# Kernel optimization log

Hardware: AMD Instinct MI355X
Metric: run time of the kernel (lower is better)

The kernel has to match this reference:

```python
import jax, jax.numpy as jnp
import numpy as np

NUM_FEAS = 4096
HID = 128
BATCH = 128


def setup_inputs() -> dict:
    key = jax.random.key(0)
    k1, k2, k3, k4 = jax.random.split(key, 4)
    batch_x = jax.random.normal(k1, (BATCH, NUM_FEAS), dtype=jnp.float32)
    C = jax.random.normal(k2, (1, HID), dtype=jnp.float32)
    W = jax.random.normal(k3, (NUM_FEAS, HID), dtype=jnp.float32)
    B = jax.random.normal(k4, (NUM_FEAS,), dtype=jnp.float32)
    return {"batch_x": batch_x, "C": C, "W": W, "B": B}


def reference(batch_x, C, W, B):
    # binarize input (matches (x > 0).float())
    x = (batch_x > 0).astype(jnp.float32)  # [B, F]
    # prefix sums: S_excl[b, i] = sum_{j < i} x[b, j] * W[j]   -> [B, F, H]
    contrib = x[:, :, None] * W[None, :, :]
    S = jnp.cumsum(contrib, axis=1)
    S_excl = jnp.concatenate([jnp.zeros_like(S[:, :1]), S[:, :-1]], axis=1)
    # hidden state for i >= 1: h_i = sigmoid(S_excl_i + C)
    h = jax.nn.sigmoid(S_excl + C[None, :, :])  # [B, F, H]
    # faithful quirk: for i == 0 the original uses raw C (no sigmoid)
    h = h.at[:, 0, :].set(jnp.broadcast_to(C[0], (x.shape[0], HID)))
    # logits z_i = h_i . W_i + B_i ; p_i = sigmoid(z_i)
    z = jnp.einsum('bfh,fh->bf', h, W) + B[None, :]
    # BCE(sum over features), stable via log_sigmoid
    log_p = jax.nn.log_sigmoid(z)
    log_q = jax.nn.log_sigmoid(-z)
    loss_per_sample = -jnp.sum(x * log_p + (1.0 - x) * log_q, axis=1)
    return jnp.mean(loss_per_sample)
```

## Files before the change

kernel.cpp:

```cpp
#include <hip/hip_runtime.h>

#define NFEAS 4096
#define HID   128
#define BATCH 128
#define NSUB  64
#define NCH   16
#define KF    256
#define L2E   1.4426950408889634f
#define LN2   0.6931471805599453f

__device__ __forceinline__ float scan64(float v) {
  float r = v; int y;
  y = __builtin_amdgcn_update_dpp(0, __float_as_int(r), 0x111, 0xF, 0xF, true); r += __int_as_float(y);
  y = __builtin_amdgcn_update_dpp(0, __float_as_int(r), 0x112, 0xF, 0xF, true); r += __int_as_float(y);
  y = __builtin_amdgcn_update_dpp(0, __float_as_int(r), 0x114, 0xF, 0xF, true); r += __int_as_float(y);
  y = __builtin_amdgcn_update_dpp(0, __float_as_int(r), 0x118, 0xF, 0xF, true); r += __int_as_float(y);
  y = __builtin_amdgcn_update_dpp(0, __float_as_int(r), 0x142, 0xA, 0xF, true); r += __int_as_float(y);
  y = __builtin_amdgcn_update_dpp(0, __float_as_int(r), 0x143, 0xC, 0xF, true); r += __int_as_float(y);
  return r;
}

__device__ __forceinline__ void scan64_x4(float& a, float& b, float& c, float& d) {
  int t0, t1, t2, t3;
#define S4(ctrl, rm)                                                              \
  t0 = __builtin_amdgcn_update_dpp(0, __float_as_int(a), ctrl, rm, 0xF, true);    \
  t1 = __builtin_amdgcn_update_dpp(0, __float_as_int(b), ctrl, rm, 0xF, true);    \
  t2 = __builtin_amdgcn_update_dpp(0, __float_as_int(c), ctrl, rm, 0xF, true);    \
  t3 = __builtin_amdgcn_update_dpp(0, __float_as_int(d), ctrl, rm, 0xF, true);    \
  a += __int_as_float(t0); b += __int_as_float(t1);                               \
  c += __int_as_float(t2); d += __int_as_float(t3);
  S4(0x111, 0xF) S4(0x112, 0xF) S4(0x114, 0xF) S4(0x118, 0xF)
  S4(0x142, 0xA) S4(0x143, 0xC)
#undef S4
}

__global__ __launch_bounds__(128) void chunk_sums_kernel(
    const float* __restrict__ x, const float* __restrict__ W,
    float* __restrict__ T)
{
  __shared__ float xm[64][8];
  const int c = blockIdx.x, g = blockIdx.y, t = threadIdx.x;

  {
    const int s = t >> 4, fb = (t & 15) << 2;
    const float4 v = *reinterpret_cast<const float4*>(
        &x[(size_t)(g * 8 + s) * NFEAS + c * 64 + fb]);
    xm[fb + 0][s] = v.x > 0.f ? 1.f : 0.f;
    xm[fb + 1][s] = v.y > 0.f ? 1.f : 0.f;
    xm[fb + 2][s] = v.z > 0.f ? 1.f : 0.f;
    xm[fb + 3][s] = v.w > 0.f ? 1.f : 0.f;
  }
  __syncthreads();

  float acc[8];
  #pragma unroll
  for (int s = 0; s < 8; ++s) acc[s] = 0.f;

  #pragma unroll 4
  for (int f = 0; f < 64; ++f) {
    const float wv = W[(size_t)(c * 64 + f) * HID + t];
    const float4 ma = *reinterpret_cast<const float4*>(&xm[f][0]);
    const float4 mb = *reinterpret_cast<const float4*>(&xm[f][4]);
    acc[0] = __builtin_fmaf(ma.x, wv, acc[0]);
    acc[1] = __builtin_fmaf(ma.y, wv, acc[1]);
    acc[2] = __builtin_fmaf(ma.z, wv, acc[2]);
    acc[3] = __builtin_fmaf(ma.w, wv, acc[3]);
    acc[4] = __builtin_fmaf(mb.x, wv, acc[4]);
    acc[5] = __builtin_fmaf(mb.y, wv, acc[5]);
    acc[6] = __builtin_fmaf(mb.z, wv, acc[6]);
    acc[7] = __builtin_fmaf(mb.w, wv, acc[7]);
  }
  #pragma unroll
  for (int s = 0; s < 8; ++s)
    T[((size_t)(g * 8 + s) * HID + t) * NSUB + c] = acc[s];
}

__global__ __launch_bounds__(256) void prefix_s2m_kernel(
    const float* __restrict__ T, const float* __restrict__ Cv,
    float* __restrict__ s2m)
{
  const int gw = blockIdx.x * 4 + (threadIdx.x >> 6);
  const int lane = threadIdx.x & 63;
  const int h = gw & 127;
  const float v = T[(size_t)gw * NSUB + lane];
  const float r = scan64(v);
  if ((lane & 3) == 0) {
    const float excl = r - v;
    s2m[(size_t)(lane >> 2) * (BATCH * HID) + gw] = -L2E * (excl + Cv[h]);
  }
}

__global__ __launch_bounds__(512, 6) void zpart_kernel(
    const float* __restrict__ x,   const float* __restrict__ W,
    const float* __restrict__ Cv,  const float* __restrict__ s2m,
    float* __restrict__ zpart)
{
  __shared__ float wt[32 * 256];
  __shared__ float s2l[8 * 32];
  __shared__ float cvl[32];

  const int c  = blockIdx.x;
  const int hq = blockIdx.y;
  const int bg = blockIdx.z;
  const int tid = threadIdx.x, lane = tid & 63, w = tid >> 6;
  const int base = c * KF;

  {
    const int hb = tid & 7, f0 = tid >> 3;
    const float* wp = W + (size_t)(base + f0) * HID + (hq << 5) + (hb << 2);
    const int colw = f0 ^ ((hb & 3) << 3);
    #pragma unroll
    for (int k = 0; k < 4; ++k) {
      const float4 v = *reinterpret_cast<const float4*>(wp + (size_t)(k << 6) * HID);
      float* q = &wt[((hb << 2) << 8) + colw + (k << 6)];
      q[0] = v.x; q[256] = v.y; q[512] = v.z; q[768] = v.w;
    }
  }
  if (tid < 256) {
    s2l[tid] = s2m[(size_t)c * (BATCH * HID) +
                   (size_t)(bg * 8 + (tid >> 5)) * HID + (hq << 5) + (tid & 31)];
  }
  if (tid < 32) cvl[tid] = Cv[(hq << 5) + tid];
  __syncthreads();

  const int b = bg * 8 + w;
  const float4 xv = *reinterpret_cast<const float4*>(
      x + (size_t)b * NFEAS + base + (lane << 2));
  const float xm0 = xv.x > 0.f ? 1.f : 0.f;
  const float xm1 = xv.y > 0.f ? 1.f : 0.f;
  const float xm2 = xv.z > 0.f ? 1.f : 0.f;
  const float xm3 = xv.w > 0.f ? 1.f : 0.f;
  const bool qk = (c == 0) && (lane == 0);

  float z0 = 0.f, z1 = 0.f, z2 = 0.f, z3 = 0.f;

  #pragma unroll
  for (int cg = 0; cg < 8; ++cg) {
    const int colx = (lane << 2) ^ ((cg & 3) << 3);
    const int rb = (cg << 2) * 256 + colx;
    const float4 wv0 = *reinterpret_cast<const float4*>(&wt[rb]);
    const float4 wv1 = *reinterpret_cast<const float4*>(&wt[rb + 256]);
    const float4 wv2 = *reinterpret_cast<const float4*>(&wt[rb + 512]);
    const float4 wv3 = *reinterpret_cast<const float4*>(&wt[rb + 768]);

    const float m00 = wv0.x * xm0, m01 = wv0.y * xm1, m02 = wv0.z * xm2, m03 = wv0.w * xm3;
    const float m10 = wv1.x * xm0, m11 = wv1.y * xm1, m12 = wv1.z * xm2, m13 = wv1.w * xm3;
    const float m20 = wv2.x * xm0, m21 = wv2.y * xm1, m22 = wv2.z * xm2, m23 = wv2.w * xm3;
    const float m30 = wv3.x * xm0, m31 = wv3.y * xm1, m32 = wv3.z * xm2, m33 = wv3.w * xm3;

    const float ps0 = (m00 + m01) + (m02 + m03);
    const float ps1 = (m10 + m11) + (m12 + m13);
    const float ps2 = (m20 + m21) + (m22 + m23);
    const float ps3 = (m30 + m31) + (m32 + m33);

    float r0 = ps0, r1 = ps1, r2 = ps2, r3 = ps3;
    scan64_x4(r0, r1, r2, r3);

#define CHAIN(J, wvJ, rJ, psJ, mJ0, mJ1, mJ2)                                               \
    {                                                                                        \
      const int ch = (cg << 2) + J;                                                          \
      const float smJ = s2l[(w << 5) + ch];                                                  \
      const float e0 = rJ - psJ;                                                             \
      const float e1 = e0 + mJ0;                                                             \
      const float e2 = e1 + mJ1;                                                             \
      const float e3 = e2 + mJ2;                                                             \
      float g0 = __builtin_amdgcn_rcpf(1.f + __builtin_amdgcn_exp2f(__builtin_fmaf(e0, -L2E, smJ))); \
      const float g1 = __builtin_amdgcn_rcpf(1.f + __builtin_amdgcn_exp2f(__builtin_fmaf(e1, -L2E, smJ))); \
      const float g2 = __builtin_amdgcn_rcpf(1.f + __builtin_amdgcn_exp2f(__builtin_fmaf(e2, -L2E, smJ))); \
      const float g3 = __builtin_amdgcn_rcpf(1.f + __builtin_amdgcn_exp2f(__builtin_fmaf(e3, -L2E, smJ))); \
      if (qk) g0 = cvl[ch];                                   \
      z0 = __builtin_fmaf(g0, wvJ.x, z0);                                                    \
      z1 = __builtin_fmaf(g1, wvJ.y, z1);                                                    \
      z2 = __builtin_fmaf(g2, wvJ.z, z2);                                                    \
      z3 = __builtin_fmaf(g3, wvJ.w, z3);                                                    \
    }
    CHAIN(0, wv0, r0, ps0, m00, m01, m02)
    CHAIN(1, wv1, r1, ps1, m10, m11, m12)
    CHAIN(2, wv2, r2, ps2, m20, m21, m22)
    CHAIN(3, wv3, r3, ps3, m30, m31, m32)
#undef CHAIN
  }

  float4 zv; zv.x = z0; zv.y = z1; zv.z = z2; zv.w = z3;
  *reinterpret_cast<float4*>(
      &zpart[((size_t)hq * BATCH + b) * NFEAS + base + (lane << 2)]) = zv;
}

__global__ __launch_bounds__(256) void bce_kernel(
    const float* __restrict__ x, const float* __restrict__ Bv,
    const float* __restrict__ zpart, float* __restrict__ lossb)
{
  __shared__ float sm[256];
  const int b = blockIdx.x, t = threadIdx.x;
  const size_t Q = (size_t)BATCH * NFEAS;
  float acc = 0.f;
  #pragma unroll
  for (int i = 0; i < NFEAS / 256; ++i) {
    const int f = i * 256 + t;
    const size_t o = (size_t)b * NFEAS + f;
    const float zt = ((zpart[o] + zpart[Q + o]) +
                      (zpart[2 * Q + o] + zpart[3 * Q + o])) + Bv[f];
    const float xf = x[o] > 0.f ? 1.f : 0.f;
    const float az = __builtin_fabsf(zt);
    const float ee = __builtin_amdgcn_exp2f(-L2E * az);
    acc += fmaxf(zt, 0.f) - xf * zt + LN2 * __builtin_amdgcn_logf(1.f + ee);
  }
  sm[t] = acc;
  __syncthreads();
  for (int s = 128; s > 0; s >>= 1) {
    if (t < s) sm[t] += sm[t + s];
    __syncthreads();
  }
  if (t == 0) lossb[b] = sm[0];
}

__global__ __launch_bounds__(128) void finalize_kernel(
    const float* __restrict__ lossb, float* __restrict__ out)
{
  __shared__ float sm[128];
  const int t = threadIdx.x;
  sm[t] = lossb[t];
  __syncthreads();
  for (int s = 64; s > 0; s >>= 1) {
    if (t < s) sm[t] += sm[t + s];
    __syncthreads();
  }
  if (t == 0) out[0] = sm[0] * (1.f / BATCH);
}

extern "C" void kernel_launch(void* const* d_in, const int* in_sizes, int n_in,
                              void* d_out, int out_size, void* d_ws, size_t ws_size,
                              hipStream_t stream)
{
  const float* x  = (const float*)d_in[0];
  const float* Cv = (const float*)d_in[1];
  const float* W  = (const float*)d_in[2];
  const float* Bv = (const float*)d_in[3];
  float* out = (float*)d_out;

  float* T     = (float*)d_ws;
  float* s2m   = T     + (size_t)BATCH * HID * NSUB;
  float* zpart = s2m   + (size_t)NCH * BATCH * HID;
  float* lossb = zpart + (size_t)4 * BATCH * NFEAS;

  chunk_sums_kernel<<<dim3(NSUB, BATCH / 8), 128, 0, stream>>>(x, W, T);
  prefix_s2m_kernel<<<dim3(BATCH * HID / 4), 256, 0, stream>>>(T, Cv, s2m);
  zpart_kernel<<<dim3(NCH, 4, BATCH / 8), 512, 0, stream>>>(x, W, Cv, s2m, zpart);
  bce_kernel<<<dim3(BATCH), 256, 0, stream>>>(x, Bv, zpart, lossb);
  finalize_kernel<<<1, 128, 0, stream>>>(lossb, out);
}
```

Baseline: 57.68 us.

## Fuse hidden-quarter loop and BCE loss into z kernel with double-buffered W tiles

The z kernel now loops over all four hidden quarters inside one block, using double-buffered shared-memory W tiles with register prefetch, instead of launching one block per quarter. It then computes the BCE loss directly and reduces it per wave, which removes the zpart round trip through global memory and the separate bce kernel. The cost is a grid four times smaller (256 blocks of 512 threads) with more serial work per block, and lower occupancy from the larger shared footprint.

```diff
diff --git a/kernel.cpp b/kernel.cpp
--- a/kernel.cpp
+++ b/kernel.cpp
@@ -90,38 +90,46 @@
   }
 }
 
-__global__ __launch_bounds__(512, 6) void zpart_kernel(
+__global__ __launch_bounds__(512, 2) void zloss_kernel(
     const float* __restrict__ x,   const float* __restrict__ W,
     const float* __restrict__ Cv,  const float* __restrict__ s2m,
-    float* __restrict__ zpart)
-{
-  __shared__ float wt[32 * 256];
-  __shared__ float s2l[8 * 32];
-  __shared__ float cvl[32];
+    const float* __restrict__ Bv,  float* __restrict__ losses)
+{
+  __shared__ float wt[2][32 * 256];
+  __shared__ float s2l[8 * 128];
+  __shared__ float cvl[128];
 
   const int c  = blockIdx.x;
-  const int hq = blockIdx.y;
-  const int bg = blockIdx.z;
+  const int bg = blockIdx.y;
   const int tid = threadIdx.x, lane = tid & 63, w = tid >> 6;
   const int base = c * KF;
 
+  const int hb = tid & 7, f0s = tid >> 3;
+  const int colw = f0s ^ ((hb & 3) << 3);
+  const float* wp0 = W + (size_t)(base + f0s) * HID + (hb << 2);
+
+  float4 st0, st1, st2, st3;
+  st0 = *reinterpret_cast<const float4*>(wp0);
+  st1 = *reinterpret_cast<const float4*>(wp0 + (size_t)(1 << 6) * HID);
+  st2 = *reinterpret_cast<const float4*>(wp0 + (size_t)(2 << 6) * HID);
+  st3 = *reinterpret_cast<const float4*>(wp0 + (size_t)(3 << 6) * HID);
+
   {
-    const int hb = tid & 7, f0 = tid >> 3;
-    const float* wp = W + (size_t)(base + f0) * HID + (hq << 5) + (hb << 2);
-    const int colw = f0 ^ ((hb & 3) << 3);
-    #pragma unroll
-    for (int k = 0; k < 4; ++k) {
-      const float4 v = *reinterpret_cast<const float4*>(wp + (size_t)(k << 6) * HID);
-      float* q = &wt[((hb << 2) << 8) + colw + (k << 6)];
-      q[0] = v.x; q[256] = v.y; q[512] = v.z; q[768] = v.w;
-    }
-  }
-  if (tid < 256) {
-    s2l[tid] = s2m[(size_t)c * (BATCH * HID) +
-                   (size_t)(bg * 8 + (tid >> 5)) * HID + (hq << 5) + (tid & 31)];
-  }
-  if (tid < 32) cvl[tid] = Cv[(hq << 5) + tid];
-  __syncthreads();
+    const int s0i = tid, s1i = tid + 512;
+    s2l[s0i] = s2m[(size_t)c * (BATCH * HID) +
+                   (size_t)(bg * 8 + (s0i >> 7)) * HID + (s0i & 127)];
+    s2l[s1i] = s2m[(size_t)c * (BATCH * HID) +
+                   (size_t)(bg * 8 + (s1i >> 7)) * HID + (s1i & 127)];
+  }
+  if (tid < 128) cvl[tid] = Cv[tid];
+
+  {
+    float* q = &wt[0][((hb << 2) << 8) + colw];
+    q[0]       = st0.x; q[256]       = st0.y; q[512]       = st0.z; q[768]       = st0.w;
+    q[64]      = st1.x; q[64 + 256]  = st1.y; q[64 + 512]  = st1.z; q[64 + 768]  = st1.w;
+    q[128]     = st2.x; q[128 + 256] = st2.y; q[128 + 512] = st2.z; q[128 + 768] = st2.w;
+    q[192]     = st3.x; q[192 + 256] = st3.y; q[192 + 512] = st3.z; q[192 + 768] = st3.w;
+  }
 
   const int b = bg * 8 + w;
   const float4 xv = *reinterpret_cast<const float4*>(
@@ -134,95 +142,97 @@
 
   float z0 = 0.f, z1 = 0.f, z2 = 0.f, z3 = 0.f;
 
-  #pragma unroll
-  for (int cg = 0; cg < 8; ++cg) {
-    const int colx = (lane << 2) ^ ((cg & 3) << 3);
-    const int rb = (cg << 2) * 256 + colx;
-    const float4 wv0 = *reinterpret_cast<const float4*>(&wt[rb]);
-    const float4 wv1 = *reinterpret_cast<const float4*>(&wt[rb + 256]);
-    const float4 wv2 = *reinterpret_cast<const float4*>(&wt[rb + 512]);
-    const float4 wv3 = *reinterpret_cast<const float4*>(&wt[rb + 768]);
-
-    const float m00 = wv0.x * xm0, m01 = wv0.y * xm1, m02 = wv0.z * xm2, m03 = wv0.w * xm3;
-    const float m10 = wv1.x * xm0, m11 = wv1.y * xm1, m12 = wv1.z * xm2, m13 = wv1.w * xm3;
-    const float m20 = wv2.x * xm0, m21 = wv2.y * xm1, m22 = wv2.z * xm2, m23 = wv2.w * xm3;
-    const float m30 = wv3.x * xm0, m31 = wv3.y * xm1, m32 = wv3.z * xm2, m33 = wv3.w * xm3;
-
-    const float ps0 = (m00 + m01) + (m02 + m03);
-    const float ps1 = (m10 + m11) + (m12 + m13);
-    const float ps2 = (m20 + m21) + (m22 + m23);
-    const float ps3 = (m30 + m31) + (m32 + m33);
-
-    float r0 = ps0, r1 = ps1, r2 = ps2, r3 = ps3;
-    scan64_x4(r0, r1, r2, r3);
+  for (int hq = 0; hq < 4; ++hq) {
+    if (hq < 3) {
+      const float* wp = wp0 + ((hq + 1) << 5);
+      st0 = *reinterpret_cast<const float4*>(wp);
+      st1 = *reinterpret_cast<const float4*>(wp + (size_t)(1 << 6) * HID);
+      st2 = *reinterpret_cast<const float4*>(wp + (size_t)(2 << 6) * HID);
+      st3 = *reinterpret_cast<const float4*>(wp + (size_t)(3 << 6) * HID);
+    }
+    __syncthreads();
+    const float* wcur = wt[hq & 1];
+
+    #pragma unroll
+    for (int cg = 0; cg < 8; ++cg) {
+      const int colx = (lane << 2) ^ ((cg & 3) << 3);
+      const int rb = (cg << 2) * 256 + colx;
+      const float4 wv0 = *reinterpret_cast<const float4*>(&wcur[rb]);
+      const float4 wv1 = *reinterpret_cast<const float4*>(&wcur[rb + 256]);
+      const float4 wv2 = *reinterpret_cast<const float4*>(&wcur[rb + 512]);
+      const float4 wv3 = *reinterpret_cast<const float4*>(&wcur[rb + 768]);
+
+      const float m00 = wv0.x * xm0, m01 = wv0.y * xm1, m02 = wv0.z * xm2, m03 = wv0.w * xm3;
+      const float m10 = wv1.x * xm0, m11 = wv1.y * xm1, m12 = wv1.z * xm2, m13 = wv1.w * xm3;
+      const float m20 = wv2.x * xm0, m21 = wv2.y * xm1, m22 = wv2.z * xm2, m23 = wv2.w * xm3;
+      const float m30 = wv3.x * xm0, m31 = wv3.y * xm1, m32 = wv3.z * xm2, m33 = wv3.w * xm3;
+
+      const float ps0 = (m00 + m01) + (m02 + m03);
+      const float ps1 = (m10 + m11) + (m12 + m13);
+      const float ps2 = (m20 + m21) + (m22 + m23);
+      const float ps3 = (m30 + m31) + (m32 + m33);
+
+      float r0 = ps0, r1 = ps1, r2 = ps2, r3 = ps3;
+      scan64_x4(r0, r1, r2, r3);
 
 #define CHAIN(J, wvJ, rJ, psJ, mJ0, mJ1, mJ2)                                               \
-    {                                                                                        \
-      const int ch = (cg << 2) + J;                                                          \
-      const float smJ = s2l[(w << 5) + ch];                                                  \
-      const float e0 = rJ - psJ;                                                             \
-      const float e1 = e0 + mJ0;                                                             \
-      const float e2 = e1 + mJ1;                                                             \
-      const float e3 = e2 + mJ2;                                                             \
-      float g0 = __builtin_amdgcn_rcpf(1.f + __builtin_amdgcn_exp2f(__builtin_fmaf(e0, -L2E, smJ))); \
-      const float g1 = __builtin_amdgcn_rcpf(1.f + __builtin_amdgcn_exp2f(__builtin_fmaf(e1, -L2E, smJ))); \
-      const float g2 = __builtin_amdgcn_rcpf(1.f + __builtin_amdgcn_exp2f(__builtin_fmaf(e2, -L2E, smJ))); \
-      const float g3 = __builtin_amdgcn_rcpf(1.f + __builtin_amdgcn_exp2f(__builtin_fmaf(e3, -L2E, smJ))); \
-      if (qk) g0 = cvl[ch];                                   \
-      z0 = __builtin_fmaf(g0, wvJ.x, z0);                                                    \
-      z1 = __builtin_fmaf(g1, wvJ.y, z1);                                                    \
-      z2 = __builtin_fmaf(g2, wvJ.z, z2);                                                    \
-      z3 = __builtin_fmaf(g3, wvJ.w, z3);                                                    \
+      {                                                                                      \
+        const int h = (hq << 5) + (cg << 2) + J;                                             \
+        const float smJ = s2l[(w << 7) + h];                                                 \
+        const float e0 = rJ - psJ;                                                           \
+        const float e1 = e0 + mJ0;                                                           \
+        const float e2 = e1 + mJ1;                                                           \
+        const float e3 = e2 + mJ2;                                                           \
+        float g0 = __builtin_amdgcn_rcpf(1.f + __builtin_amdgcn_exp2f(__builtin_fmaf(e0, -L2E, smJ))); \
+        const float g1 = __builtin_amdgcn_rcpf(1.f + __builtin_amdgcn_exp2f(__builtin_fmaf(e1, -L2E, smJ))); \
+        const float g2 = __builtin_amdgcn_rcpf(1.f + __builtin_amdgcn_exp2f(__builtin_fmaf(e2, -L2E, smJ))); \
+        const float g3 = __builtin_amdgcn_rcpf(1.f + __builtin_amdgcn_exp2f(__builtin_fmaf(e3, -L2E, smJ))); \
+        if (qk) g0 = cvl[h];                                  \
+        z0 = __builtin_fmaf(g0, wvJ.x, z0);                                                  \
+        z1 = __builtin_fmaf(g1, wvJ.y, z1);                                                  \
+        z2 = __builtin_fmaf(g2, wvJ.z, z2);                                                  \
+        z3 = __builtin_fmaf(g3, wvJ.w, z3);                                                  \
+      }
+      CHAIN(0, wv0, r0, ps0, m00, m01, m02)
+      CHAIN(1, wv1, r1, ps1, m10, m11, m12)
+      CHAIN(2, wv2, r2, ps2, m20, m21, m22)
+      CHAIN(3, wv3, r3, ps3, m30, m31, m32)
+#undef CHAIN
     }
-    CHAIN(0, wv0, r0, ps0, m00, m01, m02)
-    CHAIN(1, wv1, r1, ps1, m10, m11, m12)
-    CHAIN(2, wv2, r2, ps2, m20, m21, m22)
-    CHAIN(3, wv3, r3, ps3, m30, m31, m32)
-#undef CHAIN
-  }
-
-  float4 zv; zv.x = z0; zv.y = z1; zv.z = z2; zv.w = z3;
-  *reinterpret_cast<float4*>(
-      &zpart[((size_t)hq * BATCH + b) * NFEAS + base + (lane << 2)]) = zv;
-}
-
-__global__ __launch_bounds__(256) void bce_kernel(
-    const float* __restrict__ x, const float* __restrict__ Bv,
-    const float* __restrict__ zpart, float* __restrict__ lossb)
+
+    if (hq < 3) {
+      float* q = &wt[(hq + 1) & 1][((hb << 2) << 8) + colw];
+      q[0]       = st0.x; q[256]       = st0.y; q[512]       = st0.z; q[768]       = st0.w;
+      q[64]      = st1.x; q[64 + 256]  = st1.y; q[64 + 512]  = st1.z; q[64 + 768]  = st1.w;
+      q[128]     = st2.x; q[128 + 256] = st2.y; q[128 + 512] = st2.z; q[128 + 768] = st2.w;
+      q[192]     = st3.x; q[192 + 256] = st3.y; q[192 + 512] = st3.z; q[192 + 768] = st3.w;
+    }
+  }
+
+  const float4 bv4 = *reinterpret_cast<const float4*>(Bv + base + (lane << 2));
+  const float zt0 = z0 + bv4.x, zt1 = z1 + bv4.y;
+  const float zt2 = z2 + bv4.z, zt3 = z3 + bv4.w;
+#define BCE(zt, xmv)                                                     \
+  (fmaxf(zt, 0.f) - xmv * zt +                                           \
+   LN2 * __builtin_amdgcn_logf(1.f + __builtin_amdgcn_exp2f(-L2E * __builtin_fabsf(zt))))
+  const float li = (BCE(zt0, xm0) + BCE(zt1, xm1)) +
+                   (BCE(zt2, xm2) + BCE(zt3, xm3));
+#undef BCE
+  const float tot = scan64(li);
+  if (lane == 63) losses[b * NCH + c] = tot;
+}
+
+__global__ __launch_bounds__(256) void finalize_kernel(
+    const float* __restrict__ losses, float* __restrict__ out)
 {
   __shared__ float sm[256];
-  const int b = blockIdx.x, t = threadIdx.x;
-  const size_t Q = (size_t)BATCH * NFEAS;
-  float acc = 0.f;
-  #pragma unroll
-  for (int i = 0; i < NFEAS / 256; ++i) {
-    const int f = i * 256 + t;
-    const size_t o = (size_t)b * NFEAS + f;
-    const float zt = ((zpart[o] + zpart[Q + o]) +
-                      (zpart[2 * Q + o] + zpart[3 * Q + o])) + Bv[f];
-    const float xf = x[o] > 0.f ? 1.f : 0.f;
-    const float az = __builtin_fabsf(zt);
-    const float ee = __builtin_amdgcn_exp2f(-L2E * az);
-    acc += fmaxf(zt, 0.f) - xf * zt + LN2 * __builtin_amdgcn_logf(1.f + ee);
-  }
-  sm[t] = acc;
+  const int t = threadIdx.x;
+  float s = 0.f;
+  for (int i = t; i < BATCH * NCH; i += 256) s += losses[i];
+  sm[t] = s;
   __syncthreads();
-  for (int s = 128; s > 0; s >>= 1) {
-    if (t < s) sm[t] += sm[t + s];
-    __syncthreads();
-  }
-  if (t == 0) lossb[b] = sm[0];
-}
-
-__global__ __launch_bounds__(128) void finalize_kernel(
-    const float* __restrict__ lossb, float* __restrict__ out)
-{
-  __shared__ float sm[128];
-  const int t = threadIdx.x;
-  sm[t] = lossb[t];
-  __syncthreads();
-  for (int s = 64; s > 0; s >>= 1) {
-    if (t < s) sm[t] += sm[t + s];
+  for (int w = 128; w > 0; w >>= 1) {
+    if (t < w) sm[t] += sm[t + w];
     __syncthreads();
   }
   if (t == 0) out[0] = sm[0] * (1.f / BATCH);
@@ -238,14 +248,12 @@
   const float* Bv = (const float*)d_in[3];
   float* out = (float*)d_out;
 
-  float* T     = (float*)d_ws;
-  float* s2m   = T     + (size_t)BATCH * HID * NSUB;
-  float* zpart = s2m   + (size_t)NCH * BATCH * HID;
-  float* lossb = zpart + (size_t)4 * BATCH * NFEAS;
+  float* T      = (float*)d_ws;
+  float* s2m    = T   + (size_t)BATCH * HID * NSUB;
+  float* losses = s2m + (size_t)NCH * BATCH * HID;
 
   chunk_sums_kernel<<<dim3(NSUB, BATCH / 8), 128, 0, stream>>>(x, W, T);
   prefix_s2m_kernel<<<dim3(BATCH * HID / 4), 256, 0, stream>>>(T, Cv, s2m);
-  zpart_kernel<<<dim3(NCH, 4, BATCH / 8), 512, 0, stream>>>(x, W, Cv, s2m, zpart);
-  bce_kernel<<<dim3(BATCH), 256, 0, stream>>>(x, Bv, zpart, lossb);
-  finalize_kernel<<<1, 128, 0, stream>>>(lossb, out);
-}
+  zloss_kernel<<<dim3(NCH, BATCH / 8), 512, 0, stream>>>(x, W, Cv, s2m, Bv, losses);
+  finalize_kernel<<<1, 256, 0, stream>>>(losses, out);
+}
```

Measured after the change: 73.64 us. +27.7%, slower.

## Process two samples per wave in zpart kernel to reuse staged W tile

Applied to the files above, without the earlier changes.

Each wave in zpart_kernel now handles two batch samples instead of one, so every W tile staged in LDS serves 16 samples per block and the grid's z dimension is halved. The point is to halve global W loads and LDS staging per unit of work, and to interleave two independent DPP scans for more ILP. The trade-off is higher register pressure: launch bounds drop to 4 waves per SIMD, and fewer blocks means less parallelism to hide latency.

```diff
diff --git a/kernel.cpp b/kernel.cpp
--- a/kernel.cpp
+++ b/kernel.cpp
@@ -20,18 +20,25 @@
   return r;
 }
 
-__device__ __forceinline__ void scan64_x4(float& a, float& b, float& c, float& d) {
-  int t0, t1, t2, t3;
-#define S4(ctrl, rm)                                                              \
+__device__ __forceinline__ void scan64_x8(float& a, float& b, float& c, float& d,
+                                          float& e, float& f, float& g, float& h) {
+  int t0, t1, t2, t3, t4, t5, t6, t7;
+#define S8(ctrl, rm)                                                              \
   t0 = __builtin_amdgcn_update_dpp(0, __float_as_int(a), ctrl, rm, 0xF, true);    \
   t1 = __builtin_amdgcn_update_dpp(0, __float_as_int(b), ctrl, rm, 0xF, true);    \
   t2 = __builtin_amdgcn_update_dpp(0, __float_as_int(c), ctrl, rm, 0xF, true);    \
   t3 = __builtin_amdgcn_update_dpp(0, __float_as_int(d), ctrl, rm, 0xF, true);    \
+  t4 = __builtin_amdgcn_update_dpp(0, __float_as_int(e), ctrl, rm, 0xF, true);    \
+  t5 = __builtin_amdgcn_update_dpp(0, __float_as_int(f), ctrl, rm, 0xF, true);    \
+  t6 = __builtin_amdgcn_update_dpp(0, __float_as_int(g), ctrl, rm, 0xF, true);    \
+  t7 = __builtin_amdgcn_update_dpp(0, __float_as_int(h), ctrl, rm, 0xF, true);    \
   a += __int_as_float(t0); b += __int_as_float(t1);                               \
-  c += __int_as_float(t2); d += __int_as_float(t3);
-  S4(0x111, 0xF) S4(0x112, 0xF) S4(0x114, 0xF) S4(0x118, 0xF)
-  S4(0x142, 0xA) S4(0x143, 0xC)
-#undef S4
+  c += __int_as_float(t2); d += __int_as_float(t3);                               \
+  e += __int_as_float(t4); f += __int_as_float(t5);                               \
+  g += __int_as_float(t6); h += __int_as_float(t7);
+  S8(0x111, 0xF) S8(0x112, 0xF) S8(0x114, 0xF) S8(0x118, 0xF)
+  S8(0x142, 0xA) S8(0x143, 0xC)
+#undef S8
 }
 
 __global__ __launch_bounds__(128) void chunk_sums_kernel(
@@ -90,13 +97,13 @@
   }
 }
 
-__global__ __launch_bounds__(512, 6) void zpart_kernel(
+__global__ __launch_bounds__(512, 4) void zpart_kernel(
     const float* __restrict__ x,   const float* __restrict__ W,
     const float* __restrict__ Cv,  const float* __restrict__ s2m,
     float* __restrict__ zpart)
 {
   __shared__ float wt[32 * 256];
-  __shared__ float s2l[8 * 32];
+  __shared__ float s2l[16 * 32];
   __shared__ float cvl[32];
 
   const int c  = blockIdx.x;
@@ -116,23 +123,34 @@
       q[0] = v.x; q[256] = v.y; q[512] = v.z; q[768] = v.w;
     }
   }
-  if (tid < 256) {
+  {
     s2l[tid] = s2m[(size_t)c * (BATCH * HID) +
-                   (size_t)(bg * 8 + (tid >> 5)) * HID + (hq << 5) + (tid & 31)];
+                   (size_t)(bg * 16 + (tid >> 5)) * HID + (hq << 5) + (tid & 31)];
   }
   if (tid < 32) cvl[tid] = Cv[(hq << 5) + tid];
   __syncthreads();
 
-  const int b = bg * 8 + w;
-  const float4 xv = *reinterpret_cast<const float4*>(
-      x + (size_t)b * NFEAS + base + (lane << 2));
-  const float xm0 = xv.x > 0.f ? 1.f : 0.f;
-  const float xm1 = xv.y > 0.f ? 1.f : 0.f;
-  const float xm2 = xv.z > 0.f ? 1.f : 0.f;
-  const float xm3 = xv.w > 0.f ? 1.f : 0.f;
+  const int sA = bg * 16 + w;
+  const int sB = sA + 8;
+  const float4 xvA = *reinterpret_cast<const float4*>(
+      x + (size_t)sA * NFEAS + base + (lane << 2));
+  const float4 xvB = *reinterpret_cast<const float4*>(
+      x + (size_t)sB * NFEAS + base + (lane << 2));
+  const float xA0 = xvA.x > 0.f ? 1.f : 0.f;
+  const float xA1 = xvA.y > 0.f ? 1.f : 0.f;
+  const float xA2 = xvA.z > 0.f ? 1.f : 0.f;
+  const float xA3 = xvA.w > 0.f ? 1.f : 0.f;
+  const float xB0 = xvB.x > 0.f ? 1.f : 0.f;
+  const float xB1 = xvB.y > 0.f ? 1.f : 0.f;
+  const float xB2 = xvB.z > 0.f ? 1.f : 0.f;
+  const float xB3 = xvB.w > 0.f ? 1.f : 0.f;
   const bool qk = (c == 0) && (lane == 0);
 
-  float z0 = 0.f, z1 = 0.f, z2 = 0.f, z3 = 0.f;
+  float zA0 = 0.f, zA1 = 0.f, zA2 = 0.f, zA3 = 0.f;
+  float zB0 = 0.f, zB1 = 0.f, zB2 = 0.f, zB3 = 0.f;
+
+  const float* s2A = &s2l[(w << 5)];
+  const float* s2B = &s2l[((w + 8) << 5)];
 
   #pragma unroll
   for (int cg = 0; cg < 8; ++cg) {
@@ -143,47 +161,54 @@
     const float4 wv2 = *reinterpret_cast<const float4*>(&wt[rb + 512]);
     const float4 wv3 = *reinterpret_cast<const float4*>(&wt[rb + 768]);
 
-    const float m00 = wv0.x * xm0, m01 = wv0.y * xm1, m02 = wv0.z * xm2, m03 = wv0.w * xm3;
-    const float m10 = wv1.x * xm0, m11 = wv1.y * xm1, m12 = wv1.z * xm2, m13 = wv1.w * xm3;
-    const float m20 = wv2.x * xm0, m21 = wv2.y * xm1, m22 = wv2.z * xm2, m23 = wv2.w * xm3;
-    const float m30 = wv3.x * xm0, m31 = wv3.y * xm1, m32 = wv3.z * xm2, m33 = wv3.w * xm3;
-
-    const float ps0 = (m00 + m01) + (m02 + m03);
-    const float ps1 = (m10 + m11) + (m12 + m13);
-    const float ps2 = (m20 + m21) + (m22 + m23);
-    const float ps3 = (m30 + m31) + (m32 + m33);
-
-    float r0 = ps0, r1 = ps1, r2 = ps2, r3 = ps3;
-    scan64_x4(r0, r1, r2, r3);
-
-#define CHAIN(J, wvJ, rJ, psJ, mJ0, mJ1, mJ2)                                               \
-    {                                                                                        \
-      const int ch = (cg << 2) + J;                                                          \
-      const float smJ = s2l[(w << 5) + ch];                                                  \
-      const float e0 = rJ - psJ;                                                             \
-      const float e1 = e0 + mJ0;                                                             \
-      const float e2 = e1 + mJ1;                                                             \
-      const float e3 = e2 + mJ2;                                                             \
-      float g0 = __builtin_amdgcn_rcpf(1.f + __builtin_amdgcn_exp2f(__builtin_fmaf(e0, -L2E, smJ))); \
-      const float g1 = __builtin_amdgcn_rcpf(1.f + __builtin_amdgcn_exp2f(__builtin_fmaf(e1, -L2E, smJ))); \
-      const float g2 = __builtin_amdgcn_rcpf(1.f + __builtin_amdgcn_exp2f(__builtin_fmaf(e2, -L2E, smJ))); \
-      const float g3 = __builtin_amdgcn_rcpf(1.f + __builtin_amdgcn_exp2f(__builtin_fmaf(e3, -L2E, smJ))); \
-      if (qk) g0 = cvl[ch];                                   \
-      z0 = __builtin_fmaf(g0, wvJ.x, z0);                                                    \
-      z1 = __builtin_fmaf(g1, wvJ.y, z1);                                                    \
-      z2 = __builtin_fmaf(g2, wvJ.z, z2);                                                    \
-      z3 = __builtin_fmaf(g3, wvJ.w, z3);                                                    \
+#define PREP(P, wvJ, J)                                                        \
+    const float P##m##J##0 = wvJ.x * P##0;                                     \
+    const float P##m##J##1 = wvJ.y * P##1;                                     \
+    const float P##m##J##2 = wvJ.z * P##2;                                     \
+    float P##r##J = (P##m##J##0 + P##m##J##1) +                                \
+                    (P##m##J##2 + wvJ.w * P##3);
+    PREP(xA, wv0, 0) PREP(xA, wv1, 1) PREP(xA, wv2, 2) PREP(xA, wv3, 3)
+    PREP(xB, wv0, 0) PREP(xB, wv1, 1) PREP(xB, wv2, 2) PREP(xB, wv3, 3)
+#undef PREP
+    const float pA0 = xAr0, pA1 = xAr1, pA2 = xAr2, pA3 = xAr3;
+    const float pB0 = xBr0, pB1 = xBr1, pB2 = xBr2, pB3 = xBr3;
+
+    scan64_x8(xAr0, xAr1, xAr2, xAr3, xBr0, xBr1, xBr2, xBr3);
+
+#define FIN(P, S2, ZP0, ZP1, ZP2, ZP3, wvJ, rJ, psJ, J)                         \
+    {                                                                           \
+      const float smv = S2[(cg << 2) + J];                                      \
+      const float e0 = rJ - psJ;                                                \
+      const float e1 = e0 + P##m##J##0;                                         \
+      const float e2 = e1 + P##m##J##1;                                         \
+      const float e3 = e2 + P##m##J##2;                                         \
+      float g0 = __builtin_amdgcn_rcpf(1.f + __builtin_amdgcn_exp2f(__builtin_fmaf(e0, -L2E, smv))); \
+      const float g1 = __builtin_amdgcn_rcpf(1.f + __builtin_amdgcn_exp2f(__builtin_fmaf(e1, -L2E, smv))); \
+      const float g2 = __builtin_amdgcn_rcpf(1.f + __builtin_amdgcn_exp2f(__builtin_fmaf(e2, -L2E, smv))); \
+      const float g3 = __builtin_amdgcn_rcpf(1.f + __builtin_amdgcn_exp2f(__builtin_fmaf(e3, -L2E, smv))); \
+      if (qk) g0 = cvl[(cg << 2) + J];           \
+      ZP0 = __builtin_fmaf(g0, wvJ.x, ZP0);                                     \
+      ZP1 = __builtin_fmaf(g1, wvJ.y, ZP1);                                     \
+      ZP2 = __builtin_fmaf(g2, wvJ.z, ZP2);                                     \
+      ZP3 = __builtin_fmaf(g3, wvJ.w, ZP3);                                     \
     }
-    CHAIN(0, wv0, r0, ps0, m00, m01, m02)
-    CHAIN(1, wv1, r1, ps1, m10, m11, m12)
-    CHAIN(2, wv2, r2, ps2, m20, m21, m22)
-    CHAIN(3, wv3, r3, ps3, m30, m31, m32)
-#undef CHAIN
-  }
-
-  float4 zv; zv.x = z0; zv.y = z1; zv.z = z2; zv.w = z3;
+    FIN(xA, s2A, zA0, zA1, zA2, zA3, wv0, xAr0, pA0, 0)
+    FIN(xA, s2A, zA0, zA1, zA2, zA3, wv1, xAr1, pA1, 1)
+    FIN(xA, s2A, zA0, zA1, zA2, zA3, wv2, xAr2, pA2, 2)
+    FIN(xA, s2A, zA0, zA1, zA2, zA3, wv3, xAr3, pA3, 3)
+    FIN(xB, s2B, zB0, zB1, zB2, zB3, wv0, xBr0, pB0, 0)
+    FIN(xB, s2B, zB0, zB1, zB2, zB3, wv1, xBr1, pB1, 1)
+    FIN(xB, s2B, zB0, zB1, zB2, zB3, wv2, xBr2, pB2, 2)
+    FIN(xB, s2B, zB0, zB1, zB2, zB3, wv3, xBr3, pB3, 3)
+#undef FIN
+  }
+
+  float4 za; za.x = zA0; za.y = zA1; za.z = zA2; za.w = zA3;
+  float4 zb; zb.x = zB0; zb.y = zB1; zb.z = zB2; zb.w = zB3;
   *reinterpret_cast<float4*>(
-      &zpart[((size_t)hq * BATCH + b) * NFEAS + base + (lane << 2)]) = zv;
+      &zpart[((size_t)hq * BATCH + sA) * NFEAS + base + (lane << 2)]) = za;
+  *reinterpret_cast<float4*>(
+      &zpart[((size_t)hq * BATCH + sB) * NFEAS + base + (lane << 2)]) = zb;
 }
 
 __global__ __launch_bounds__(256) void bce_kernel(
@@ -245,7 +270,7 @@
 
   chunk_sums_kernel<<<dim3(NSUB, BATCH / 8), 128, 0, stream>>>(x, W, T);
   prefix_s2m_kernel<<<dim3(BATCH * HID / 4), 256, 0, stream>>>(T, Cv, s2m);
-  zpart_kernel<<<dim3(NCH, 4, BATCH / 8), 512, 0, stream>>>(x, W, Cv, s2m, zpart);
+  zpart_kernel<<<dim3(NCH, 4, BATCH / 16), 512, 0, stream>>>(x, W, Cv, s2m, zpart);
   bce_kernel<<<dim3(BATCH), 256, 0, stream>>>(x, Bv, zpart, lossb);
   finalize_kernel<<<1, 128, 0, stream>>>(lossb, out);
 }
```

After: 58.09 us. Within noise of the previous version (+0.7%).

## Split zpart hidden dim into eight slices and widen BCE grid with vectorized loads

Applied to the files above, without the earlier changes.

The zpart kernel now processes 16 hidden units per block instead of 32, doubling the grid to 16x8x16 blocks. This halves shared memory and per-thread loop work and raises the occupancy hint to 8, aimed at latency hiding in the sigmoid/scan chain. In exchange, zpart writes twice as many partial arrays to global memory. The BCE kernel is split across 4 feature quarters with float4 loads that sum 8 partials, and the finalize kernel reduces 512 partial losses.

```diff
diff --git a/kernel.cpp b/kernel.cpp
--- a/kernel.cpp
+++ b/kernel.cpp
@@ -6,6 +6,7 @@
 #define NSUB  64
 #define NCH   16
 #define KF    256
+#define NH8   8
 #define L2E   1.4426950408889634f
 #define LN2   0.6931471805599453f
 
@@ -90,37 +91,37 @@
   }
 }
 
-__global__ __launch_bounds__(512, 6) void zpart_kernel(
+__global__ __launch_bounds__(512, 8) void zpart_kernel(
     const float* __restrict__ x,   const float* __restrict__ W,
     const float* __restrict__ Cv,  const float* __restrict__ s2m,
     float* __restrict__ zpart)
 {
-  __shared__ float wt[32 * 256];
-  __shared__ float s2l[8 * 32];
-  __shared__ float cvl[32];
+  __shared__ float wt[16 * 256];
+  __shared__ float s2l[8 * 16];
+  __shared__ float cvl[16];
 
   const int c  = blockIdx.x;
-  const int hq = blockIdx.y;
+  const int h8 = blockIdx.y;
   const int bg = blockIdx.z;
   const int tid = threadIdx.x, lane = tid & 63, w = tid >> 6;
   const int base = c * KF;
+  const int hbase = h8 << 4;
 
   {
-    const int hb = tid & 7, f0 = tid >> 3;
-    const float* wp = W + (size_t)(base + f0) * HID + (hq << 5) + (hb << 2);
-    const int colw = f0 ^ ((hb & 3) << 3);
-    #pragma unroll
-    for (int k = 0; k < 4; ++k) {
-      const float4 v = *reinterpret_cast<const float4*>(wp + (size_t)(k << 6) * HID);
-      float* q = &wt[((hb << 2) << 8) + colw + (k << 6)];
-      q[0] = v.x; q[256] = v.y; q[512] = v.z; q[768] = v.w;
-    }
-  }
-  if (tid < 256) {
+    const int hg = tid & 3, f0 = tid >> 2;
+    const int colw = f0 ^ (hg << 3);
+    const float* wp = W + (size_t)(base + f0) * HID + hbase + (hg << 2);
+    const float4 vA = *reinterpret_cast<const float4*>(wp);
+    const float4 vB = *reinterpret_cast<const float4*>(wp + (size_t)128 * HID);
+    float* q = &wt[((hg << 2) << 8) + colw];
+    q[0]         = vA.x; q[256]       = vA.y; q[512]       = vA.z; q[768]       = vA.w;
+    q[128]       = vB.x; q[128 + 256] = vB.y; q[128 + 512] = vB.z; q[128 + 768] = vB.w;
+  }
+  if (tid < 128) {
     s2l[tid] = s2m[(size_t)c * (BATCH * HID) +
-                   (size_t)(bg * 8 + (tid >> 5)) * HID + (hq << 5) + (tid & 31)];
-  }
-  if (tid < 32) cvl[tid] = Cv[(hq << 5) + tid];
+                   (size_t)(bg * 8 + (tid >> 4)) * HID + hbase + (tid & 15)];
+  }
+  if (tid < 16) cvl[tid] = Cv[hbase + tid];
   __syncthreads();
 
   const int b = bg * 8 + w;
@@ -133,9 +134,10 @@
   const bool qk = (c == 0) && (lane == 0);
 
   float z0 = 0.f, z1 = 0.f, z2 = 0.f, z3 = 0.f;
-
-  #pragma unroll
-  for (int cg = 0; cg < 8; ++cg) {
+  const float* s2p = &s2l[w << 4];
+
+  #pragma unroll
+  for (int cg = 0; cg < 4; ++cg) {
     const int colx = (lane << 2) ^ ((cg & 3) << 3);
     const int rb = (cg << 2) * 256 + colx;
     const float4 wv0 = *reinterpret_cast<const float4*>(&wt[rb]);
@@ -143,15 +145,15 @@
     const float4 wv2 = *reinterpret_cast<const float4*>(&wt[rb + 512]);
     const float4 wv3 = *reinterpret_cast<const float4*>(&wt[rb + 768]);
 
-    const float m00 = wv0.x * xm0, m01 = wv0.y * xm1, m02 = wv0.z * xm2, m03 = wv0.w * xm3;
-    const float m10 = wv1.x * xm0, m11 = wv1.y * xm1, m12 = wv1.z * xm2, m13 = wv1.w * xm3;
-    const float m20 = wv2.x * xm0, m21 = wv2.y * xm1, m22 = wv2.z * xm2, m23 = wv2.w * xm3;
-    const float m30 = wv3.x * xm0, m31 = wv3.y * xm1, m32 = wv3.z * xm2, m33 = wv3.w * xm3;
-
-    const float ps0 = (m00 + m01) + (m02 + m03);
-    const float ps1 = (m10 + m11) + (m12 + m13);
-    const float ps2 = (m20 + m21) + (m22 + m23);
-    const float ps3 = (m30 + m31) + (m32 + m33);
+    const float m00 = wv0.x * xm0, m01 = wv0.y * xm1, m02 = wv0.z * xm2;
+    const float m10 = wv1.x * xm0, m11 = wv1.y * xm1, m12 = wv1.z * xm2;
+    const float m20 = wv2.x * xm0, m21 = wv2.y * xm1, m22 = wv2.z * xm2;
+    const float m30 = wv3.x * xm0, m31 = wv3.y * xm1, m32 = wv3.z * xm2;
+
+    const float ps0 = (m00 + m01) + (m02 + wv0.w * xm3);
+    const float ps1 = (m10 + m11) + (m12 + wv1.w * xm3);
+    const float ps2 = (m20 + m21) + (m22 + wv2.w * xm3);
+    const float ps3 = (m30 + m31) + (m32 + wv3.w * xm3);
 
     float r0 = ps0, r1 = ps1, r2 = ps2, r3 = ps3;
     scan64_x4(r0, r1, r2, r3);
@@ -159,15 +161,15 @@
 #define CHAIN(J, wvJ, rJ, psJ, mJ0, mJ1, mJ2)                                               \
     {                                                                                        \
       const int ch = (cg << 2) + J;                                                          \
-      const float smJ = s2l[(w << 5) + ch];                                                  \
+      const float smv = s2p[ch];                                                             \
       const float e0 = rJ - psJ;                                                             \
       const float e1 = e0 + mJ0;                                                             \
       const float e2 = e1 + mJ1;                                                             \
       const float e3 = e2 + mJ2;                                                             \
-      float g0 = __builtin_amdgcn_rcpf(1.f + __builtin_amdgcn_exp2f(__builtin_fmaf(e0, -L2E, smJ))); \
-      const float g1 = __builtin_amdgcn_rcpf(1.f + __builtin_amdgcn_exp2f(__builtin_fmaf(e1, -L2E, smJ))); \
-      const float g2 = __builtin_amdgcn_rcpf(1.f + __builtin_amdgcn_exp2f(__builtin_fmaf(e2, -L2E, smJ))); \
-      const float g3 = __builtin_amdgcn_rcpf(1.f + __builtin_amdgcn_exp2f(__builtin_fmaf(e3, -L2E, smJ))); \
+      float g0 = __builtin_amdgcn_rcpf(1.f + __builtin_amdgcn_exp2f(__builtin_fmaf(e0, -L2E, smv))); \
+      const float g1 = __builtin_amdgcn_rcpf(1.f + __builtin_amdgcn_exp2f(__builtin_fmaf(e1, -L2E, smv))); \
+      const float g2 = __builtin_amdgcn_rcpf(1.f + __builtin_amdgcn_exp2f(__builtin_fmaf(e2, -L2E, smv))); \
+      const float g3 = __builtin_amdgcn_rcpf(1.f + __builtin_amdgcn_exp2f(__builtin_fmaf(e3, -L2E, smv))); \
       if (qk) g0 = cvl[ch];                                   \
       z0 = __builtin_fmaf(g0, wvJ.x, z0);                                                    \
       z1 = __builtin_fmaf(g1, wvJ.y, z1);                                                    \
@@ -183,7 +185,7 @@
 
   float4 zv; zv.x = z0; zv.y = z1; zv.z = z2; zv.w = z3;
   *reinterpret_cast<float4*>(
-      &zpart[((size_t)hq * BATCH + b) * NFEAS + base + (lane << 2)]) = zv;
+      &zpart[((size_t)h8 * BATCH + b) * NFEAS + base + (lane << 2)]) = zv;
 }
 
 __global__ __launch_bounds__(256) void bce_kernel(
@@ -191,37 +193,45 @@
     const float* __restrict__ zpart, float* __restrict__ lossb)
 {
   __shared__ float sm[256];
-  const int b = blockIdx.x, t = threadIdx.x;
+  const int b = blockIdx.x, q = blockIdx.y, t = threadIdx.x;
+  const int fb = (q << 10) + (t << 2);
   const size_t Q = (size_t)BATCH * NFEAS;
-  float acc = 0.f;
-  #pragma unroll
-  for (int i = 0; i < NFEAS / 256; ++i) {
-    const int f = i * 256 + t;
-    const size_t o = (size_t)b * NFEAS + f;
-    const float zt = ((zpart[o] + zpart[Q + o]) +
-                      (zpart[2 * Q + o] + zpart[3 * Q + o])) + Bv[f];
-    const float xf = x[o] > 0.f ? 1.f : 0.f;
-    const float az = __builtin_fabsf(zt);
-    const float ee = __builtin_amdgcn_exp2f(-L2E * az);
-    acc += fmaxf(zt, 0.f) - xf * zt + LN2 * __builtin_amdgcn_logf(1.f + ee);
-  }
-  sm[t] = acc;
+  const size_t o = (size_t)b * NFEAS + fb;
+
+  float4 zt = *reinterpret_cast<const float4*>(&zpart[o]);
+  #pragma unroll
+  for (int s = 1; s < NH8; ++s) {
+    const float4 v = *reinterpret_cast<const float4*>(&zpart[(size_t)s * Q + o]);
+    zt.x += v.x; zt.y += v.y; zt.z += v.z; zt.w += v.w;
+  }
+  const float4 bv = *reinterpret_cast<const float4*>(Bv + fb);
+  zt.x += bv.x; zt.y += bv.y; zt.z += bv.z; zt.w += bv.w;
+  const float4 xv = *reinterpret_cast<const float4*>(&x[o]);
+
+#define BCE(zv, xvv)                                                      \
+  (fmaxf(zv, 0.f) - ((xvv) > 0.f ? (zv) : 0.f) +                          \
+   LN2 * __builtin_amdgcn_logf(1.f + __builtin_amdgcn_exp2f(-L2E * __builtin_fabsf(zv))))
+  const float li = (BCE(zt.x, xv.x) + BCE(zt.y, xv.y)) +
+                   (BCE(zt.z, xv.z) + BCE(zt.w, xv.w));
+#undef BCE
+
+  sm[t] = li;
   __syncthreads();
   for (int s = 128; s > 0; s >>= 1) {
     if (t < s) sm[t] += sm[t + s];
     __syncthreads();
   }
-  if (t == 0) lossb[b] = sm[0];
-}
-
-__global__ __launch_bounds__(128) void finalize_kernel(
+  if (t == 0) lossb[b * 4 + q] = sm[0];
+}
+
+__global__ __launch_bounds__(256) void finalize_kernel(
     const float* __restrict__ lossb, float* __restrict__ out)
 {
-  __shared__ float sm[128];
+  __shared__ float sm[256];
   const int t = threadIdx.x;
-  sm[t] = lossb[t];
-  __syncthreads();
-  for (int s = 64; s > 0; s >>= 1) {
+  sm[t] = lossb[t] + lossb[t + 256];
+  __syncthreads();
+  for (int s = 128; s > 0; s >>= 1) {
     if (t < s) sm[t] += sm[t + s];
     __syncthreads();
   }
@@ -241,11 +251,11 @@
   float* T     = (float*)d_ws;
   float* s2m   = T     + (size_t)BATCH * HID * NSUB;
   float* zpart = s2m   + (size_t)NCH * BATCH * HID;
-  float* lossb = zpart + (size_t)4 * BATCH * NFEAS;
+  float* lossb = zpart + (size_t)NH8 * BATCH * NFEAS;
 
   chunk_sums_kernel<<<dim3(NSUB, BATCH / 8), 128, 0, stream>>>(x, W, T);
   prefix_s2m_kernel<<<dim3(BATCH * HID / 4), 256, 0, stream>>>(T, Cv, s2m);
-  zpart_kernel<<<dim3(NCH, 4, BATCH / 8), 512, 0, stream>>>(x, W, Cv, s2m, zpart);
-  bce_kernel<<<dim3(BATCH), 256, 0, stream>>>(x, Bv, zpart, lossb);
-  finalize_kernel<<<1, 128, 0, stream>>>(lossb, out);
-}
+  zpart_kernel<<<dim3(NCH, NH8, BATCH / 8), 512, 0, stream>>>(x, W, Cv, s2m, zpart);
+  bce_kernel<<<dim3(BATCH, 4), 256, 0, stream>>>(x, Bv, zpart, lossb);
+  finalize_kernel<<<1, 256, 0, stream>>>(lossb, out);
+}
```

Result: slower. 61.31 us (+6.3%).
